# Kernel tuning notes

Measured on AMD Instinct MI355X. Metric: run time of the kernel, lower is better.

Reference implementation:

```python
import jax, jax.numpy as jnp
import numpy as np

D_STATE = 64
D_CONV = 4
DT_RANK = 16  # ceil(256/16)
LN_EPS = 1e-5


def _mamba_layer(x, ln_g, ln_b, in_w, conv_w, conv_b, xp_w, dt_w, dt_b, A_log, Dp, out_w):
    B, L, d_model = x.shape
    # LayerNorm (pre-norm)
    mu = x.mean(-1, keepdims=True)
    var = ((x - mu) ** 2).mean(-1, keepdims=True)
    xn = (x - mu) * jax.lax.rsqrt(var + LN_EPS) * ln_g + ln_b
    # in_proj -> split into x-branch and gate z
    xz = xn @ in_w.T                    # [B,L,2*d_inner]
    xm, z = jnp.split(xz, 2, axis=-1)   # each [B,L,d_inner]
    d_inner = xm.shape[-1]
    # causal depthwise conv1d (kernel D_CONV), then SiLU
    xp = jnp.pad(xm, ((0, 0), (D_CONV - 1, 0), (0, 0)))
    xc = conv_b + sum(xp[:, k:k + L, :] * conv_w[:, k] for k in range(D_CONV))
    xc = jax.nn.silu(xc)
    # input-dependent SSM params
    dbl = xc @ xp_w.T                   # [B,L,dt_rank+2*N]
    dt, Bm, Cm = jnp.split(dbl, [DT_RANK, DT_RANK + D_STATE], axis=-1)
    dt = jax.nn.softplus(dt @ dt_w.T + dt_b)   # [B,L,d_inner]
    A = -jnp.exp(A_log)                 # [d_inner, N]

    def step(h, inp):
        dt_t, B_t, C_t, u_t = inp       # [B,Di],[B,N],[B,N],[B,Di]
        dA = jnp.exp(dt_t[:, :, None] * A)                 # [B,Di,N]
        dBu = (dt_t * u_t)[:, :, None] * B_t[:, None, :]   # [B,Di,N]
        h = dA * h + dBu
        y = jnp.einsum('bdn,bn->bd', h, C_t)
        return h, y

    h0 = jnp.zeros((B, d_inner, D_STATE), x.dtype)
    _, ys = jax.lax.scan(
        step, h0,
        (dt.transpose(1, 0, 2), Bm.transpose(1, 0, 2), Cm.transpose(1, 0, 2), xc.transpose(1, 0, 2)))
    y = ys.transpose(1, 0, 2) + xc * Dp  # skip term D*u
    y = y * jax.nn.silu(z)               # gating
    out = y @ out_w.T                    # out_proj
    return out + x                       # residual


def reference(x, ln_g, ln_b, in_w, conv_w, conv_b, xp_w, dt_w, dt_b, A_log, Dp, out_w):
    depth = ln_g.shape[0]
    for i in range(depth):
        x = _mamba_layer(x, ln_g[i], ln_b[i], in_w[i], conv_w[i], conv_b[i],
                         xp_w[i], dt_w[i], dt_b[i], A_log[i], Dp[i], out_w[i])
    return x


def setup_inputs() -> dict:
    key = jax.random.key(0)
    ks = jax.random.split(key, 8)
    B, L, d_model, depth = 4, 1024, 256, 2
    d_inner = 2 * d_model
    x = jax.random.normal(ks[0], (B, L, d_model), jnp.float32)
    s = 0.02
    in_w = jax.random.normal(ks[1], (depth, 2 * d_inner, d_model), jnp.float32) * s
    conv_w = jax.random.normal(ks[2], (depth, d_inner, D_CONV), jnp.float32) * 0.3
    conv_b = jnp.zeros((depth, d_inner), jnp.float32)
    xp_w = jax.random.normal(ks[3], (depth, DT_RANK + 2 * D_STATE, d_inner), jnp.float32) * s
    dt_w = jax.random.normal(ks[4], (depth, d_inner, DT_RANK), jnp.float32) * 0.1
    # inverse-softplus of ~0.01 so dt starts small (mamba-style init)
    dt_b = jnp.full((depth, d_inner), float(np.log(np.expm1(0.01))), jnp.float32)
    # A = diag(1..N) per channel -> A_log = log(arange)
    A_log = jnp.broadcast_to(jnp.log(jnp.arange(1, D_STATE + 1, dtype=jnp.float32)),
                             (depth, d_inner, D_STATE))
    Dp = jnp.ones((depth, d_inner), jnp.float32)
    out_w = jax.random.normal(ks[5], (depth, d_model, d_inner), jnp.float32) * s
    ln_g = jnp.ones((depth, d_model), jnp.float32)
    ln_b = jnp.zeros((depth, d_model), jnp.float32)
    return {"x": x, "ln_g": ln_g, "ln_b": ln_b, "in_w": in_w, "conv_w": conv_w,
            "conv_b": conv_b, "xp_w": xp_w, "dt_w": dt_w, "dt_b": dt_b,
            "A_log": A_log, "Dp": Dp, "out_w": out_w}
```

## Files before the change

### kernel.cpp

```cpp
#include <hip/hip_runtime.h>
#include <math.h>

#define DI 512
#define DM 256
#define LSEQ 1024
#define BB 4
#define NST 64
#define ROWS (BB*LSEQ)
#define NC 16
#define CL 64

typedef __bf16 bf16x8 __attribute__((ext_vector_type(8)));
typedef __bf16 bf16x4 __attribute__((ext_vector_type(4)));
typedef float f32x4 __attribute__((ext_vector_type(4)));
typedef unsigned short u16;
typedef u16 u16x8 __attribute__((ext_vector_type(8)));
typedef int i32x2 __attribute__((ext_vector_type(2)));

__device__ __forceinline__ float siluf(float x) { return x / (1.f + __expf(-x)); }
__device__ __forceinline__ float softplusf(float x) { return (x > 20.f) ? x : log1pf(__expf(x)); }
__device__ __forceinline__ float rlane(float v, int l) {
    return __int_as_float(__builtin_amdgcn_readlane(__float_as_int(v), l));
}
__device__ __forceinline__ float fexp2(float x) {
#if __has_builtin(__builtin_amdgcn_exp2f)
    return __builtin_amdgcn_exp2f(x);
#else
    return __expf(x * 0.69314718056f);
#endif
}
__device__ __forceinline__ float bf2f(u16 u) {
    return __uint_as_float(((unsigned)u) << 16);
}
template<int PAT>
__device__ __forceinline__ float fswz(float v) {
    return __int_as_float(__builtin_amdgcn_ds_swizzle(__float_as_int(v), PAT));
}

__device__ __forceinline__ float tree8(const float (&s)[8], int lane) {
    const bool b4 = (lane & 16) != 0;
    const bool b3 = (lane & 8) != 0;
    float r[4];
#if __has_builtin(__builtin_amdgcn_permlane32_swap)
    #pragma unroll
    for (int i = 0; i < 4; ++i) {
        i32x2 pr = __builtin_amdgcn_permlane32_swap(
            __float_as_int(s[i]), __float_as_int(s[i+4]), false, false);
        r[i] = __int_as_float(pr[0]) + __int_as_float(pr[1]);
    }
#else
    const bool b5 = (lane & 32) != 0;
    #pragma unroll
    for (int i = 0; i < 4; ++i) {
        float u = b5 ? s[i+4] : s[i];
        float w = b5 ? s[i]   : s[i+4];
        r[i] = u + __shfl_xor(w, 32, 64);
    }
#endif
    float q[2];
    #pragma unroll
    for (int i = 0; i < 2; ++i) {
        float u = b4 ? r[i+2] : r[i];
        float w = b4 ? r[i]   : r[i+2];
        q[i] = u + fswz<0x401F>(w);
    }
    float u = b3 ? q[1] : q[0];
    float w = b3 ? q[0] : q[1];
    float p = u + fswz<0x201F>(w);
    p += fswz<0x101F>(p);
    p += fswz<0x081F>(p);
    p += fswz<0x041F>(p);
    return p;
}

__global__ __launch_bounds__(256) void f2bf3(
    const float* __restrict__ a, __bf16* __restrict__ da, int na,
    const float* __restrict__ b, __bf16* __restrict__ db, int nb,
    const float* __restrict__ c, __bf16* __restrict__ dc, int nc)
{
    int i = (blockIdx.x * 256 + threadIdx.x) * 4;
    const float* src; __bf16* dst;
    if (i < na) { src = a + i; dst = da + i; }
    else {
        i -= na;
        if (i < nb) { src = b + i; dst = db + i; }
        else {
            i -= nb;
            if (i >= nc) return;
            src = c + i; dst = dc + i;
        }
    }
    float4 v = *(const float4*)src;
    bf16x4 o;
    o[0] = (__bf16)v.x; o[1] = (__bf16)v.y; o[2] = (__bf16)v.z; o[3] = (__bf16)v.w;
    *(bf16x4*)dst = o;
}

__global__ __launch_bounds__(256) void ln_kernel(
    const float* __restrict__ x, const float* __restrict__ g,
    const float* __restrict__ b, __bf16* __restrict__ xn)
{
    int lane = threadIdx.x & 63;
    int row = blockIdx.x * 4 + (threadIdx.x >> 6);
    const float4* xr = (const float4*)(x + (size_t)row * DM);
    float4 v = xr[lane];
    float s = v.x + v.y + v.z + v.w;
    #pragma unroll
    for (int o = 32; o; o >>= 1) s += __shfl_xor(s, o, 64);
    float mu = s * (1.f / DM);
    float dx = v.x - mu, dy = v.y - mu, dz = v.z - mu, dw = v.w - mu;
    float q = dx*dx + dy*dy + dz*dz + dw*dw;
    #pragma unroll
    for (int o = 32; o; o >>= 1) q += __shfl_xor(q, o, 64);
    float inv = rsqrtf(q * (1.f / DM) + 1e-5f);
    float4 gv = ((const float4*)g)[lane];
    float4 bv = ((const float4*)b)[lane];
    bf16x4 o4;
    o4[0] = (__bf16)(dx * inv * gv.x + bv.x);
    o4[1] = (__bf16)(dy * inv * gv.y + bv.y);
    o4[2] = (__bf16)(dz * inv * gv.z + bv.z);
    o4[3] = (__bf16)(dw * inv * gv.w + bv.w);
    *(bf16x4*)(xn + (size_t)row * DM + lane * 4) = o4;
}

template<int KK>
__global__ __launch_bounds__(256) void gemm_mfma(
    const __bf16* __restrict__ A, const __bf16* __restrict__ W,
    float* __restrict__ C, __bf16* __restrict__ C1b, __bf16* __restrict__ C2b,
    const float* __restrict__ res, int N, int mode)
{
    int wid = threadIdx.x >> 6, lane = threadIdx.x & 63;
    int wr = wid >> 1, wc = wid & 1;
    int bm = blockIdx.y * 64, bn = blockIdx.x * 64;
    int l15 = lane & 15, lk = (lane >> 4) * 8;
    const __bf16* Ap = A + (size_t)(bm + wr*32 + l15) * KK + lk;
    int wrow0 = bn + wc*32 + l15;
    int wrow1 = wrow0 + 16;
    if (wrow0 > N-1) wrow0 = N-1;
    if (wrow1 > N-1) wrow1 = N-1;
    const __bf16* Wp0 = W + (size_t)wrow0 * KK + lk;
    const __bf16* Wp1 = W + (size_t)wrow1 * KK + lk;
    f32x4 acc[2][2] = {};
    #pragma unroll 4
    for (int k0 = 0; k0 < KK; k0 += 32) {
        bf16x8 b0 = *(const bf16x8*)(Wp0 + k0);
        bf16x8 b1 = *(const bf16x8*)(Wp1 + k0);
        #pragma unroll
        for (int m = 0; m < 2; ++m) {
            bf16x8 a = *(const bf16x8*)(Ap + (size_t)m*16*KK + k0);
            acc[m][0] = __builtin_amdgcn_mfma_f32_16x16x32_bf16(a, b0, acc[m][0], 0, 0, 0);
            acc[m][1] = __builtin_amdgcn_mfma_f32_16x16x32_bf16(a, b1, acc[m][1], 0, 0, 0);
        }
    }
    int r4 = (lane >> 4) * 4;
    #pragma unroll
    for (int m = 0; m < 2; ++m) {
        int row = bm + wr*32 + m*16 + r4;
        #pragma unroll
        for (int n = 0; n < 2; ++n) {
            int col = bn + wc*32 + n*16 + l15;
            #pragma unroll
            for (int r = 0; r < 4; ++r) {
                float v = acc[m][n][r];
                int rr = row + r;
                if (mode == 0) {
                    if (col < N) C[(size_t)rr * N + col] = v;
                } else if (mode == 1) {
                    if (col < 512) C1b[(size_t)rr * 512 + col] = (__bf16)v;
                    else           C2b[(size_t)rr * 512 + col - 512] = (__bf16)v;
                } else {
                    C[(size_t)rr * N + col] = v + res[(size_t)rr * N + col];
                }
            }
        }
    }
}

__global__ __launch_bounds__(256) void gemm_dt(
    const float* __restrict__ A, int lda,
    const float* __restrict__ W,
    float* __restrict__ CT, const float* __restrict__ aux)
{
    __shared__ float As[16][68];
    __shared__ float Ws[16][68];
    __shared__ float Ct[64][66];
    const int bm = blockIdx.y * 64;
    const int bn = blockIdx.x * 64;
    const int tid = threadIdx.x;
    const int tx = tid & 15;
    const int ty = tid >> 4;
    const int lr = tid >> 2;
    const int lc = (tid & 3) << 2;
    float acc[4][4] = {};
    {
        float4 av = *(const float4*)(A + (size_t)(bm + lr) * lda + lc);
        float4 wv = *(const float4*)(W + (size_t)(bn + lr) * 16 + lc);
        As[lc+0][lr] = av.x; As[lc+1][lr] = av.y; As[lc+2][lr] = av.z; As[lc+3][lr] = av.w;
        Ws[lc+0][lr] = wv.x; Ws[lc+1][lr] = wv.y; Ws[lc+2][lr] = wv.z; Ws[lc+3][lr] = wv.w;
        __syncthreads();
        #pragma unroll
        for (int k = 0; k < 16; ++k) {
            float a[4], w[4];
            #pragma unroll
            for (int i = 0; i < 4; ++i) a[i] = As[k][ty*4 + i];
            #pragma unroll
            for (int j = 0; j < 4; ++j) w[j] = Ws[k][tx*4 + j];
            #pragma unroll
            for (int i = 0; i < 4; ++i)
                #pragma unroll
                for (int j = 0; j < 4; ++j)
                    acc[i][j] = fmaf(a[i], w[j], acc[i][j]);
        }
    }
    #pragma unroll
    for (int j = 0; j < 4; ++j) {
        float bia = aux[bn + tx*4 + j];
        #pragma unroll
        for (int i = 0; i < 4; ++i)
            Ct[tx*4 + j][ty*4 + i] = softplusf(acc[i][j] + bia);
    }
    __syncthreads();
    {
        int n = tid >> 2;
        int mc = (tid & 3) * 16;
        float* dst = CT + (size_t)(bn + n) * ROWS + bm + mc;
        #pragma unroll
        for (int j4 = 0; j4 < 4; ++j4) {
            float4 v;
            v.x = Ct[n][mc + j4*4 + 0];
            v.y = Ct[n][mc + j4*4 + 1];
            v.z = Ct[n][mc + j4*4 + 2];
            v.w = Ct[n][mc + j4*4 + 3];
            *(float4*)(dst + j4*4) = v;
        }
    }
}

__global__ __launch_bounds__(256) void conv_tr_kernel(
    const __bf16* __restrict__ xm, const float* __restrict__ cw,
    const float* __restrict__ cb, const u16* __restrict__ zin,
    __bf16* __restrict__ xcb, u16* __restrict__ xcT, u16* __restrict__ zT)
{
    __shared__ float xs[67][66];
    __shared__ u16 Tc[64][72];
    __shared__ u16 Tz[64][72];
    const int tid = threadIdx.x;
    const int row0 = blockIdx.y * 64;
    const int d0 = blockIdx.x * 64;
    #pragma unroll
    for (int it = 0; it < 3; ++it) {
        int q = it * 256 + tid;
        if (q < 67 * 8) {
            int rr = q >> 3;
            int cc = (q & 7) * 8;
            int g = row0 - 3 + rr;
            float f[8] = {0.f,0.f,0.f,0.f,0.f,0.f,0.f,0.f};
            if (g >= 0 && (g >> 10) == (row0 >> 10)) {
                u16x8 v = *(const u16x8*)((const u16*)xm + (size_t)g * DI + d0 + cc);
                #pragma unroll
                for (int j = 0; j < 8; ++j) f[j] = bf2f(v[j]);
            }
            #pragma unroll
            for (int j = 0; j < 8; ++j) xs[rr][cc + j] = f[j];
        }
    }
    const int r = tid >> 2;
    const int c0 = (tid & 3) * 16;
    {
        const u16* zp = zin + (size_t)(row0 + r) * DI + d0 + c0;
        *(u16x8*)&Tz[r][c0]     = *(const u16x8*)(zp);
        *(u16x8*)&Tz[r][c0 + 8] = *(const u16x8*)(zp + 8);
    }
    __syncthreads();
    {
        bf16x8 v0, v1;
        #pragma unroll
        for (int j = 0; j < 16; ++j) {
            int d = d0 + c0 + j;
            float acc = cb[d]
                + xs[r+0][c0+j] * cw[d*4+0]
                + xs[r+1][c0+j] * cw[d*4+1]
                + xs[r+2][c0+j] * cw[d*4+2]
                + xs[r+3][c0+j] * cw[d*4+3];
            __bf16 o = (__bf16)siluf(acc);
            if (j < 8) v0[j] = o; else v1[j-8] = o;
            Tc[r][c0+j] = *(const u16*)&o;
        }
        __bf16* op = xcb + (size_t)(row0 + r) * DI + d0 + c0;
        *(bf16x8*)(op)     = v0;
        *(bf16x8*)(op + 8) = v1;
    }
    __syncthreads();
    {
        u16x8 a0, a1, b0, b1;
        #pragma unroll
        for (int i = 0; i < 8; ++i) {
            a0[i] = Tc[c0+i][r];   a1[i] = Tc[c0+8+i][r];
            b0[i] = Tz[c0+i][r];   b1[i] = Tz[c0+8+i][r];
        }
        u16* oc = xcT + (size_t)(d0 + r) * ROWS + row0 + c0;
        u16* oz = zT  + (size_t)(d0 + r) * ROWS + row0 + c0;
        *(u16x8*)(oc)     = a0;
        *(u16x8*)(oc + 8) = a1;
        *(u16x8*)(oz)     = b0;
        *(u16x8*)(oz + 8) = b1;
    }
}

__global__ __launch_bounds__(256) void transpose_bf(
    const u16* __restrict__ in, u16* __restrict__ out, int ldi, int ldo)
{
    __shared__ u16 tile[64][72];
    int r = threadIdx.x >> 2;
    int c0 = (threadIdx.x & 3) * 16;
    const u16* ip = in + (size_t)(blockIdx.y*64 + r) * ldi + blockIdx.x*64 + c0;
    *(u16x8*)&tile[r][c0]     = *(const u16x8*)(ip);
    *(u16x8*)&tile[r][c0 + 8] = *(const u16x8*)(ip + 8);
    __syncthreads();
    u16* op = out + (size_t)(blockIdx.x*64 + r) * ldo + blockIdx.y*64 + c0;
    u16x8 v0, v1;
    #pragma unroll
    for (int i = 0; i < 8; ++i) { v0[i] = tile[c0+i][r]; v1[i] = tile[c0+8+i][r]; }
    *(u16x8*)(op)     = v0;
    *(u16x8*)(op + 8) = v1;
}

__global__ __launch_bounds__(256) void scan_fused2(
    const float* __restrict__ dtT, const __bf16* __restrict__ xcT,
    const __bf16* __restrict__ zT, const float* __restrict__ dbl,
    const float* __restrict__ A_log, const float* __restrict__ Dp,
    __bf16* __restrict__ yT)
{
    __shared__ float Pa[12][NST];
    __shared__ float Ha[12][NST];
    __shared__ float Ys[4][64];
    const int w = threadIdx.x >> 6;
    const int lane = threadIdx.x & 63;
    const int d = blockIdx.x & (DI - 1);
    const int b = blockIdx.x >> 9;
    const float An2 = -__expf(A_log[d * NST + lane]) * 1.44269504f;
    const float dpd = Dp[d];
    const size_t rowb = (size_t)b * LSEQ;
    const size_t tixb = (size_t)d * ROWS + rowb;

    #pragma unroll 1
    for (int cc = 0; cc < 3; ++cc) {
        const int c = w * 3 + cc;
        const size_t tix = tixb + (size_t)c * CL;
        float dtv = dtT[tix + lane];
        float uvf = (float)xcT[tix + lane];
        float duv = dtv * uvf;
        float Sdt = dtv;
        #pragma unroll
        for (int o = 32; o; o >>= 1) Sdt += __shfl_xor(Sdt, o, 64);
        const float* bp = dbl + (rowb + (size_t)c * CL) * 144 + 16 + lane;
        float H = 0.f;
        #pragma unroll
        for (int j = 0; j < 8; ++j) {
            #pragma unroll
            for (int q = 0; q < 8; ++q) {
                const int t = 8*j + q;
                float dA = fexp2(rlane(dtv, t) * An2);
                H = fmaf(dA, H, rlane(duv, t) * bp[q * 144]);
            }
            bp += 8 * 144;
        }
        Pa[c][lane] = fexp2(An2 * Sdt);
        Ha[c][lane] = H;
    }
    __syncthreads();

    float h = 0.f;
    #pragma unroll 1
    for (int j = 0; j < w * 4; ++j)
        h = fmaf(Pa[j][lane], h, Ha[j][lane]);

    #pragma unroll 1
    for (int cc = 0; cc < 4; ++cc) {
        const int c = w * 4 + cc;
        const size_t tix = tixb + (size_t)c * CL;
        float dtv = dtT[tix + lane];
        float uvf = (float)xcT[tix + lane];
        float zvf = (float)zT[tix + lane];
        float duv = dtv * uvf;
        float gD  = uvf * dpd;
        float wz  = siluf(zvf);
        const float* bp = dbl + (rowb + (size_t)c * CL) * 144 + 16 + lane;
        const float* cp = bp + 64;
        float yred[8];
        #pragma unroll
        for (int j = 0; j < 8; ++j) {
            float s[8];
            #pragma unroll
            for (int q = 0; q < 8; ++q) {
                const int t = 8*j + q;
                float dA = fexp2(rlane(dtv, t) * An2);
                h = fmaf(dA, h, rlane(duv, t) * bp[q * 144]);
                s[q] = h * cp[q * 144];
            }
            yred[j] = tree8(s, lane);
            bp += 8 * 144;
            cp += 8 * 144;
        }
        if ((lane & 7) == 0) {
            #pragma unroll
            for (int j = 0; j < 8; ++j) Ys[w][8*j + (lane >> 3)] = yred[j];
        }
        float y = (Ys[w][lane] + gD) * wz;
        yT[tix + lane] = (__bf16)y;
    }
}

extern "C" void kernel_launch(void* const* d_in, const int* in_sizes, int n_in,
                              void* d_out, int out_size, void* d_ws, size_t ws_size,
                              hipStream_t stream)
{
    const float* x      = (const float*)d_in[0];
    const float* ln_g   = (const float*)d_in[1];
    const float* ln_b   = (const float*)d_in[2];
    const float* in_w   = (const float*)d_in[3];
    const float* conv_w = (const float*)d_in[4];
    const float* conv_b = (const float*)d_in[5];
    const float* xp_w   = (const float*)d_in[6];
    const float* dt_w   = (const float*)d_in[7];
    const float* dt_b   = (const float*)d_in[8];
    const float* A_log  = (const float*)d_in[9];
    const float* Dp     = (const float*)d_in[10];
    const float* out_w  = (const float*)d_in[11];
    float* out = (float*)d_out;

    char* ws = (char*)d_ws;
    const size_t MB = 1u << 20;
    __bf16* xmb  = (__bf16*)(ws + 0*MB);
    float*  dtT  = (float*)(ws + 8*MB);
    __bf16* xcbf = (__bf16*)(ws + 16*MB);
    __bf16* yTb  = (__bf16*)(ws + 16*MB);
    __bf16* xcT  = (__bf16*)(ws + 20*MB);
    __bf16* zbf  = (__bf16*)(ws + 24*MB);
    __bf16* ybf  = (__bf16*)(ws + 24*MB);
    __bf16* zT   = (__bf16*)(ws + 28*MB);
    float*  dblb = (float*)(ws + 40*MB);
    __bf16* xnb  = (__bf16*)(ws + 43*MB);
    __bf16* w_in  = (__bf16*)(ws + 45*MB);
    __bf16* w_xp  = (__bf16*)(ws + 46*MB);
    __bf16* w_out = (__bf16*)(ws + 46*MB + 512*1024);

    const int na = 2*1024*DM, nb = 2*144*DI, nc = 2*DM*DI;
    f2bf3<<<(na+nb+nc)/1024, 256, 0, stream>>>(
        in_w, w_in, na, xp_w, w_xp, nb, out_w, w_out, nc);

    for (int l = 0; l < 2; ++l) {
        const float* xin = (l == 0) ? x : out;
        ln_kernel<<<ROWS/4, 256, 0, stream>>>(xin, ln_g + l*DM, ln_b + l*DM, xnb);
        gemm_mfma<DM><<<dim3(1024/64, ROWS/64), 256, 0, stream>>>(
            xnb, w_in + (size_t)l*1024*DM, nullptr, xmb, zbf, nullptr, 1024, 1);
        conv_tr_kernel<<<dim3(DI/64, ROWS/64), 256, 0, stream>>>(
            xmb, conv_w + (size_t)l*DI*4, conv_b + (size_t)l*DI,
            (const u16*)zbf, xcbf, (u16*)xcT, (u16*)zT);
        gemm_mfma<DI><<<dim3(3, ROWS/64), 256, 0, stream>>>(
            xcbf, w_xp + (size_t)l*144*DI, dblb, nullptr, nullptr, nullptr, 144, 0);
        gemm_dt<<<dim3(DI/64, ROWS/64), 256, 0, stream>>>(
            dblb, 144, dt_w + (size_t)l*DI*16, dtT, dt_b + (size_t)l*DI);
        scan_fused2<<<BB*DI, 256, 0, stream>>>(
            dtT, xcT, zT, dblb, A_log + (size_t)l*DI*NST, Dp + (size_t)l*DI, yTb);
        transpose_bf<<<dim3(ROWS/64, DI/64), 256, 0, stream>>>(
            (const u16*)yTb, (u16*)ybf, ROWS, DI);
        gemm_mfma<DI><<<dim3(DM/64, ROWS/64), 256, 0, stream>>>(
            ybf, w_out + (size_t)l*DM*DI, out, nullptr, nullptr, xin, DM, 2);
    }
}
```

Measured before the change: 289.8 us.

## Fold dt projection into x_proj weights and fuse transpose into out_proj GEMM

Precomputes a combined dt_w·xp_w[:16] weight (512x512) so dt comes straight from xc in one MFMA GEMM, which also produces B/C in the same launch. This removes the separate fp32 gemm_dt kernel and the dbl round-trip for dt. The out_proj GEMM now reads the transposed scan output directly through an LDS transpose, which eliminates the separate transpose kernel. The cost is a larger dt GEMM (K=512 instead of 16), bf16 rounding of the folded weight, and an extra syncthreads per K-step in the out GEMM.

```diff
diff --git a/kernel.cpp b/kernel.cpp
--- a/kernel.cpp
+++ b/kernel.cpp
@@ -96,6 +96,22 @@
     *(bf16x4*)dst = o;
 }
 
+__global__ __launch_bounds__(256) void wdt_prep(
+    const float* __restrict__ dt_w, const float* __restrict__ xp_w,
+    __bf16* __restrict__ wde)
+{
+    int idx = blockIdx.x * 256 + threadIdx.x;
+    int k = idx & 511;
+    int o = (idx >> 9) & 511;
+    int l = idx >> 18;
+    const float* dw = dt_w + ((size_t)l*512 + o) * 16;
+    const float* xw = xp_w + (size_t)l*144*512 + k;
+    float s = 0.f;
+    #pragma unroll
+    for (int r = 0; r < 16; ++r) s += dw[r] * xw[(size_t)r*512];
+    wde[idx] = (__bf16)s;
+}
+
 __global__ __launch_bounds__(256) void ln_kernel(
     const float* __restrict__ x, const float* __restrict__ g,
     const float* __restrict__ b, __bf16* __restrict__ xn)
@@ -124,10 +140,9 @@
 }
 
 template<int KK>
-__global__ __launch_bounds__(256) void gemm_mfma(
+__global__ __launch_bounds__(256) void gemm_mfma_split(
     const __bf16* __restrict__ A, const __bf16* __restrict__ W,
-    float* __restrict__ C, __bf16* __restrict__ C1b, __bf16* __restrict__ C2b,
-    const float* __restrict__ res, int N, int mode)
+    __bf16* __restrict__ C1b, __bf16* __restrict__ C2b)
 {
     int wid = threadIdx.x >> 6, lane = threadIdx.x & 63;
     int wr = wid >> 1, wc = wid & 1;
@@ -135,11 +150,8 @@
     int l15 = lane & 15, lk = (lane >> 4) * 8;
     const __bf16* Ap = A + (size_t)(bm + wr*32 + l15) * KK + lk;
     int wrow0 = bn + wc*32 + l15;
-    int wrow1 = wrow0 + 16;
-    if (wrow0 > N-1) wrow0 = N-1;
-    if (wrow1 > N-1) wrow1 = N-1;
     const __bf16* Wp0 = W + (size_t)wrow0 * KK + lk;
-    const __bf16* Wp1 = W + (size_t)wrow1 * KK + lk;
+    const __bf16* Wp1 = Wp0 + (size_t)16 * KK;
     f32x4 acc[2][2] = {};
     #pragma unroll 4
     for (int k0 = 0; k0 < KK; k0 += 32) {
@@ -163,74 +175,81 @@
             for (int r = 0; r < 4; ++r) {
                 float v = acc[m][n][r];
                 int rr = row + r;
-                if (mode == 0) {
-                    if (col < N) C[(size_t)rr * N + col] = v;
-                } else if (mode == 1) {
-                    if (col < 512) C1b[(size_t)rr * 512 + col] = (__bf16)v;
-                    else           C2b[(size_t)rr * 512 + col - 512] = (__bf16)v;
-                } else {
-                    C[(size_t)rr * N + col] = v + res[(size_t)rr * N + col];
-                }
-            }
-        }
-    }
-}
-
-__global__ __launch_bounds__(256) void gemm_dt(
-    const float* __restrict__ A, int lda,
-    const float* __restrict__ W,
-    float* __restrict__ CT, const float* __restrict__ aux)
-{
-    __shared__ float As[16][68];
-    __shared__ float Ws[16][68];
+                if (col < 512) C1b[(size_t)rr * 512 + col] = (__bf16)v;
+                else           C2b[(size_t)rr * 512 + col - 512] = (__bf16)v;
+            }
+        }
+    }
+}
+
+__global__ __launch_bounds__(256) void gemm_xpdt(
+    const __bf16* __restrict__ A,
+    const __bf16* __restrict__ Wbc,
+    const __bf16* __restrict__ Wdt,
+    float* __restrict__ dblBC, float* __restrict__ dtT,
+    const float* __restrict__ dt_b)
+{
     __shared__ float Ct[64][66];
-    const int bm = blockIdx.y * 64;
-    const int bn = blockIdx.x * 64;
-    const int tid = threadIdx.x;
-    const int tx = tid & 15;
-    const int ty = tid >> 4;
-    const int lr = tid >> 2;
-    const int lc = (tid & 3) << 2;
-    float acc[4][4] = {};
-    {
-        float4 av = *(const float4*)(A + (size_t)(bm + lr) * lda + lc);
-        float4 wv = *(const float4*)(W + (size_t)(bn + lr) * 16 + lc);
-        As[lc+0][lr] = av.x; As[lc+1][lr] = av.y; As[lc+2][lr] = av.z; As[lc+3][lr] = av.w;
-        Ws[lc+0][lr] = wv.x; Ws[lc+1][lr] = wv.y; Ws[lc+2][lr] = wv.z; Ws[lc+3][lr] = wv.w;
+    const int bx = blockIdx.x;
+    const bool isdt = bx >= 2;
+    const int bn = isdt ? (bx - 2) * 64 : bx * 64;
+    const __bf16* W = isdt ? Wdt : Wbc;
+    int wid = threadIdx.x >> 6, lane = threadIdx.x & 63;
+    int wr = wid >> 1, wc = wid & 1;
+    int bm = blockIdx.y * 64;
+    int l15 = lane & 15, lk = (lane >> 4) * 8;
+    const __bf16* Ap = A + (size_t)(bm + wr*32 + l15) * DI + lk;
+    const __bf16* Wp0 = W + (size_t)(bn + wc*32 + l15) * DI + lk;
+    const __bf16* Wp1 = Wp0 + (size_t)16 * DI;
+    f32x4 acc[2][2] = {};
+    #pragma unroll 4
+    for (int k0 = 0; k0 < DI; k0 += 32) {
+        bf16x8 b0 = *(const bf16x8*)(Wp0 + k0);
+        bf16x8 b1 = *(const bf16x8*)(Wp1 + k0);
+        #pragma unroll
+        for (int m = 0; m < 2; ++m) {
+            bf16x8 a = *(const bf16x8*)(Ap + (size_t)m*16*DI + k0);
+            acc[m][0] = __builtin_amdgcn_mfma_f32_16x16x32_bf16(a, b0, acc[m][0], 0, 0, 0);
+            acc[m][1] = __builtin_amdgcn_mfma_f32_16x16x32_bf16(a, b1, acc[m][1], 0, 0, 0);
+        }
+    }
+    int r4 = (lane >> 4) * 4;
+    if (!isdt) {
+        #pragma unroll
+        for (int m = 0; m < 2; ++m) {
+            int row = bm + wr*32 + m*16 + r4;
+            #pragma unroll
+            for (int n = 0; n < 2; ++n) {
+                int col = bn + wc*32 + n*16 + l15;
+                #pragma unroll
+                for (int r = 0; r < 4; ++r)
+                    dblBC[(size_t)(row + r) * 128 + col] = acc[m][n][r];
+            }
+        }
+    } else {
+        #pragma unroll
+        for (int m = 0; m < 2; ++m) {
+            int rl = wr*32 + m*16 + r4;
+            #pragma unroll
+            for (int n = 0; n < 2; ++n) {
+                int cl = wc*32 + n*16 + l15;
+                float bia = dt_b[bn + cl];
+                #pragma unroll
+                for (int r = 0; r < 4; ++r)
+                    Ct[cl][rl + r] = softplusf(acc[m][n][r] + bia);
+            }
+        }
         __syncthreads();
-        #pragma unroll
-        for (int k = 0; k < 16; ++k) {
-            float a[4], w[4];
-            #pragma unroll
-            for (int i = 0; i < 4; ++i) a[i] = As[k][ty*4 + i];
-            #pragma unroll
-            for (int j = 0; j < 4; ++j) w[j] = Ws[k][tx*4 + j];
-            #pragma unroll
-            for (int i = 0; i < 4; ++i)
-                #pragma unroll
-                for (int j = 0; j < 4; ++j)
-                    acc[i][j] = fmaf(a[i], w[j], acc[i][j]);
-        }
-    }
-    #pragma unroll
-    for (int j = 0; j < 4; ++j) {
-        float bia = aux[bn + tx*4 + j];
-        #pragma unroll
-        for (int i = 0; i < 4; ++i)
-            Ct[tx*4 + j][ty*4 + i] = softplusf(acc[i][j] + bia);
-    }
-    __syncthreads();
-    {
-        int n = tid >> 2;
-        int mc = (tid & 3) * 16;
-        float* dst = CT + (size_t)(bn + n) * ROWS + bm + mc;
+        int nr = threadIdx.x >> 2;
+        int mc = (threadIdx.x & 3) * 16;
+        float* dst = dtT + (size_t)(bn + nr) * ROWS + bm + mc;
         #pragma unroll
         for (int j4 = 0; j4 < 4; ++j4) {
             float4 v;
-            v.x = Ct[n][mc + j4*4 + 0];
-            v.y = Ct[n][mc + j4*4 + 1];
-            v.z = Ct[n][mc + j4*4 + 2];
-            v.w = Ct[n][mc + j4*4 + 3];
+            v.x = Ct[nr][mc + j4*4 + 0];
+            v.y = Ct[nr][mc + j4*4 + 1];
+            v.z = Ct[nr][mc + j4*4 + 2];
+            v.w = Ct[nr][mc + j4*4 + 3];
             *(float4*)(dst + j4*4) = v;
         }
     }
@@ -307,27 +326,9 @@
     }
 }
 
-__global__ __launch_bounds__(256) void transpose_bf(
-    const u16* __restrict__ in, u16* __restrict__ out, int ldi, int ldo)
-{
-    __shared__ u16 tile[64][72];
-    int r = threadIdx.x >> 2;
-    int c0 = (threadIdx.x & 3) * 16;
-    const u16* ip = in + (size_t)(blockIdx.y*64 + r) * ldi + blockIdx.x*64 + c0;
-    *(u16x8*)&tile[r][c0]     = *(const u16x8*)(ip);
-    *(u16x8*)&tile[r][c0 + 8] = *(const u16x8*)(ip + 8);
-    __syncthreads();
-    u16* op = out + (size_t)(blockIdx.x*64 + r) * ldo + blockIdx.y*64 + c0;
-    u16x8 v0, v1;
-    #pragma unroll
-    for (int i = 0; i < 8; ++i) { v0[i] = tile[c0+i][r]; v1[i] = tile[c0+8+i][r]; }
-    *(u16x8*)(op)     = v0;
-    *(u16x8*)(op + 8) = v1;
-}
-
 __global__ __launch_bounds__(256) void scan_fused2(
     const float* __restrict__ dtT, const __bf16* __restrict__ xcT,
-    const __bf16* __restrict__ zT, const float* __restrict__ dbl,
+    const __bf16* __restrict__ zT, const float* __restrict__ dblBC,
     const float* __restrict__ A_log, const float* __restrict__ Dp,
     __bf16* __restrict__ yT)
 {
@@ -353,7 +354,7 @@
         float Sdt = dtv;
         #pragma unroll
         for (int o = 32; o; o >>= 1) Sdt += __shfl_xor(Sdt, o, 64);
-        const float* bp = dbl + (rowb + (size_t)c * CL) * 144 + 16 + lane;
+        const float* bp = dblBC + (rowb + (size_t)c * CL) * 128 + lane;
         float H = 0.f;
         #pragma unroll
         for (int j = 0; j < 8; ++j) {
@@ -361,9 +362,9 @@
             for (int q = 0; q < 8; ++q) {
                 const int t = 8*j + q;
                 float dA = fexp2(rlane(dtv, t) * An2);
-                H = fmaf(dA, H, rlane(duv, t) * bp[q * 144]);
-            }
-            bp += 8 * 144;
+                H = fmaf(dA, H, rlane(duv, t) * bp[q * 128]);
+            }
+            bp += 8 * 128;
         }
         Pa[c][lane] = fexp2(An2 * Sdt);
         Ha[c][lane] = H;
@@ -385,7 +386,7 @@
         float duv = dtv * uvf;
         float gD  = uvf * dpd;
         float wz  = siluf(zvf);
-        const float* bp = dbl + (rowb + (size_t)c * CL) * 144 + 16 + lane;
+        const float* bp = dblBC + (rowb + (size_t)c * CL) * 128 + lane;
         const float* cp = bp + 64;
         float yred[8];
         #pragma unroll
@@ -395,12 +396,12 @@
             for (int q = 0; q < 8; ++q) {
                 const int t = 8*j + q;
                 float dA = fexp2(rlane(dtv, t) * An2);
-                h = fmaf(dA, h, rlane(duv, t) * bp[q * 144]);
-                s[q] = h * cp[q * 144];
+                h = fmaf(dA, h, rlane(duv, t) * bp[q * 128]);
+                s[q] = h * cp[q * 128];
             }
             yred[j] = tree8(s, lane);
-            bp += 8 * 144;
-            cp += 8 * 144;
+            bp += 8 * 128;
+            cp += 8 * 128;
         }
         if ((lane & 7) == 0) {
             #pragma unroll
@@ -408,6 +409,52 @@
         }
         float y = (Ys[w][lane] + gD) * wz;
         yT[tix + lane] = (__bf16)y;
+    }
+}
+
+__global__ __launch_bounds__(256) void gemm_outT(
+    const __bf16* __restrict__ AT, const __bf16* __restrict__ W,
+    float* __restrict__ C, const float* __restrict__ res)
+{
+    __shared__ u16 At[64][40];
+    const int tid = threadIdx.x;
+    int wid = tid >> 6, lane = tid & 63;
+    int wr = wid >> 1, wc = wid & 1;
+    int bm = blockIdx.y * 64, bn = blockIdx.x * 64;
+    int l15 = lane & 15, lk = (lane >> 4) * 8;
+    const __bf16* Wp0 = W + (size_t)(bn + wc*32 + l15) * DI + lk;
+    const __bf16* Wp1 = Wp0 + (size_t)16 * DI;
+    const int kr = tid >> 3;
+    const int mc = (tid & 7) * 8;
+    f32x4 acc[2][2] = {};
+    for (int k0 = 0; k0 < DI; k0 += 32) {
+        u16x8 av = *(const u16x8*)((const u16*)AT + (size_t)(k0 + kr) * ROWS + bm + mc);
+        bf16x8 b0 = *(const bf16x8*)(Wp0 + k0);
+        bf16x8 b1 = *(const bf16x8*)(Wp1 + k0);
+        __syncthreads();
+        #pragma unroll
+        for (int j = 0; j < 8; ++j) At[mc + j][kr] = av[j];
+        __syncthreads();
+        #pragma unroll
+        for (int m = 0; m < 2; ++m) {
+            bf16x8 a = *(const bf16x8*)&At[wr*32 + m*16 + l15][lk];
+            acc[m][0] = __builtin_amdgcn_mfma_f32_16x16x32_bf16(a, b0, acc[m][0], 0, 0, 0);
+            acc[m][1] = __builtin_amdgcn_mfma_f32_16x16x32_bf16(a, b1, acc[m][1], 0, 0, 0);
+        }
+    }
+    int r4 = (lane >> 4) * 4;
+    #pragma unroll
+    for (int m = 0; m < 2; ++m) {
+        int row = bm + wr*32 + m*16 + r4;
+        #pragma unroll
+        for (int n = 0; n < 2; ++n) {
+            int col = bn + wc*32 + n*16 + l15;
+            #pragma unroll
+            for (int r = 0; r < 4; ++r) {
+                int rr = row + r;
+                C[(size_t)rr * DM + col] = acc[m][n][r] + res[(size_t)rr * DM + col];
+            }
+        }
     }
 }
 
@@ -437,35 +484,33 @@
     __bf16* yTb  = (__bf16*)(ws + 16*MB);
     __bf16* xcT  = (__bf16*)(ws + 20*MB);
     __bf16* zbf  = (__bf16*)(ws + 24*MB);
-    __bf16* ybf  = (__bf16*)(ws + 24*MB);
     __bf16* zT   = (__bf16*)(ws + 28*MB);
-    float*  dblb = (float*)(ws + 40*MB);
+    float*  dblBC= (float*)(ws + 32*MB);
     __bf16* xnb  = (__bf16*)(ws + 43*MB);
     __bf16* w_in  = (__bf16*)(ws + 45*MB);
     __bf16* w_xp  = (__bf16*)(ws + 46*MB);
     __bf16* w_out = (__bf16*)(ws + 46*MB + 512*1024);
-
-    const int na = 2*1024*DM, nb = 2*144*DI, nc = 2*DM*DI;
-    f2bf3<<<(na+nb+nc)/1024, 256, 0, stream>>>(
-        in_w, w_in, na, xp_w, w_xp, nb, out_w, w_out, nc);
+    __bf16* w_de  = (__bf16*)(ws + 48*MB);
+
+    const int na = 2*1024*DM, nb = 2*144*DI, ncv = 2*DM*DI;
+    f2bf3<<<(na+nb+ncv)/1024, 256, 0, stream>>>(
+        in_w, w_in, na, xp_w, w_xp, nb, out_w, w_out, ncv);
+    wdt_prep<<<(2*512*512)/256, 256, 0, stream>>>(dt_w, xp_w, w_de);
 
     for (int l = 0; l < 2; ++l) {
         const float* xin = (l == 0) ? x : out;
         ln_kernel<<<ROWS/4, 256, 0, stream>>>(xin, ln_g + l*DM, ln_b + l*DM, xnb);
-        gemm_mfma<DM><<<dim3(1024/64, ROWS/64), 256, 0, stream>>>(
-            xnb, w_in + (size_t)l*1024*DM, nullptr, xmb, zbf, nullptr, 1024, 1);
+        gemm_mfma_split<DM><<<dim3(1024/64, ROWS/64), 256, 0, stream>>>(
+            xnb, w_in + (size_t)l*1024*DM, xmb, zbf);
         conv_tr_kernel<<<dim3(DI/64, ROWS/64), 256, 0, stream>>>(
             xmb, conv_w + (size_t)l*DI*4, conv_b + (size_t)l*DI,
             (const u16*)zbf, xcbf, (u16*)xcT, (u16*)zT);
-        gemm_mfma<DI><<<dim3(3, ROWS/64), 256, 0, stream>>>(
-            xcbf, w_xp + (size_t)l*144*DI, dblb, nullptr, nullptr, nullptr, 144, 0);
-        gemm_dt<<<dim3(DI/64, ROWS/64), 256, 0, stream>>>(
-            dblb, 144, dt_w + (size_t)l*DI*16, dtT, dt_b + (size_t)l*DI);
+        gemm_xpdt<<<dim3(10, ROWS/64), 256, 0, stream>>>(
+            xcbf, w_xp + (size_t)l*144*DI + 16*DI, w_de + (size_t)l*DI*DI,
+            dblBC, dtT, dt_b + (size_t)l*DI);
         scan_fused2<<<BB*DI, 256, 0, stream>>>(
-            dtT, xcT, zT, dblb, A_log + (size_t)l*DI*NST, Dp + (size_t)l*DI, yTb);
-        transpose_bf<<<dim3(ROWS/64, DI/64), 256, 0, stream>>>(
-            (const u16*)yTb, (u16*)ybf, ROWS, DI);
-        gemm_mfma<DI><<<dim3(DM/64, ROWS/64), 256, 0, stream>>>(
-            ybf, w_out + (size_t)l*DM*DI, out, nullptr, nullptr, xin, DM, 2);
-    }
-}
+            dtT, xcT, zT, dblBC, A_log + (size_t)l*DI*NST, Dp + (size_t)l*DI, yTb);
+        gemm_outT<<<dim3(DM/64, ROWS/64), 256, 0, stream>>>(
+            yTb, w_out + (size_t)l*DM*DI, out, xin);
+    }
+}
```

Measured after the change: 296.5 us. +2.3%, slower.
